# Performance work log

Measured on AMD Instinct MI355X. Metric: run time of the kernel, lower is better.

The kernel has to match this reference:

```python
import jax, jax.numpy as jnp
import numpy as np

N = 100_000   # nodes
E = 1_250_000 # edges
D = 64        # node feature dim
H = 64        # hidden_channels
C = 10        # num_classes
G = 128       # graphs in batch


def setup_inputs() -> dict:
    key = jax.random.key(0)
    ks = jax.random.split(key, 12)
    x = jax.random.normal(ks[0], (N, D), dtype=jnp.float32)
    edge_index = jax.random.randint(ks[1], (2, E), 0, N, dtype=jnp.int64)
    batch = jnp.sort(jax.random.randint(ks[2], (N,), 0, G, dtype=jnp.int64))
    s = lambda fan_in: 1.0 / np.sqrt(fan_in)
    W1 = jax.random.normal(ks[3], (D, H), dtype=jnp.float32) * s(D)
    b1 = jnp.zeros((H,), dtype=jnp.float32)
    W2 = jax.random.normal(ks[4], (H, H), dtype=jnp.float32) * s(H)
    b2 = jnp.zeros((H,), dtype=jnp.float32)
    W3 = jax.random.normal(ks[5], (H, H), dtype=jnp.float32) * s(H)
    b3 = jnp.zeros((H,), dtype=jnp.float32)
    Wl = jax.random.normal(ks[6], (H, C), dtype=jnp.float32) * s(H)
    bl = jnp.zeros((C,), dtype=jnp.float32)
    return {"x": x, "edge_index": edge_index, "batch": batch,
            "W1": W1, "b1": b1, "W2": W2, "b2": b2,
            "W3": W3, "b3": b3, "Wl": Wl, "bl": bl}


def _gcn_conv(h, W, b, src, dst, norm, n_nodes):
    # GCNConv: out[i] = sum_{e: dst(e)=i} norm_e * (h @ W)[src(e)] + b
    h = h @ W
    msg = h[src] * norm[:, None]                       # [E+N, H]
    return jax.ops.segment_sum(msg, dst, num_segments=n_nodes) + b


def reference(x, edge_index, batch, W1, b1, W2, b2, W3, b3, Wl, bl):
    x = x.astype(jnp.float32)
    ei = edge_index.astype(jnp.int64)
    # add self-loops (as PyG gcn_norm does by default)
    loop = jnp.arange(N, dtype=ei.dtype)
    src = jnp.concatenate([ei[0], loop])
    dst = jnp.concatenate([ei[1], loop])
    # symmetric normalization: deg over targets (in-degree incl. self-loops)
    deg = jax.ops.segment_sum(jnp.ones_like(src, dtype=jnp.float32), dst,
                              num_segments=N)
    dinv = jnp.where(deg > 0, jax.lax.rsqrt(jnp.maximum(deg, 1.0)), 0.0)
    norm = dinv[src] * dinv[dst]                       # [E+N]

    h = jax.nn.relu(_gcn_conv(x, W1, b1, src, dst, norm, N))
    h = jax.nn.relu(_gcn_conv(h, W2, b2, src, dst, norm, N))
    h = _gcn_conv(h, W3, b3, src, dst, norm, N)

    # global_mean_pool over graph ids
    ones = jnp.ones((N,), dtype=jnp.float32)
    counts = jax.ops.segment_sum(ones, batch, num_segments=G)
    sums = jax.ops.segment_sum(h, batch, num_segments=G)
    pooled = sums / jnp.maximum(counts, 1.0)[:, None]  # [G, H]

    # dropout is identity in eval mode
    return pooled @ Wl + bl                            # [G, C]
```

## Files before the change

kernel.cpp:

```cpp
#include <hip/hip_runtime.h>
#include <hip/hip_bf16.h>


#define BSHIFT 7
#define BNODES (1 << BSHIFT)
#define EPB    8192
#define MAXDEG 8192
#define MAXBUCKET 32768

typedef __attribute__((ext_vector_type(8))) short bf16x8;
typedef __attribute__((ext_vector_type(4))) float f32x4;

__device__ __forceinline__ void atomAddF(float* p, float v) {
#if defined(__gfx90a__) || defined(__gfx940__) || defined(__gfx941__) || defined(__gfx942__) || defined(__gfx950__)
    unsafeAtomicAdd(p, v);
#else
    atomicAdd(p, v);
#endif
}

__device__ __forceinline__ unsigned short f2bf(float x) {
    unsigned u = __float_as_uint(x);
    u += 0x7FFFu + ((u >> 16) & 1u);
    return (unsigned short)(u >> 16);
}
__device__ __forceinline__ float bf2f(unsigned short b) {
    return __uint_as_float((unsigned)b << 16);
}

__global__ __launch_bounds__(256)
void k_bhist(const int* __restrict__ dst, int* __restrict__ cnt_all,
             int nE, int nBuckets, int binBlocks,
             const float* __restrict__ W1, const float* __restrict__ W2,
             const float* __restrict__ W3, unsigned short* __restrict__ Wt) {
    if (blockIdx.x >= binBlocks) {
        int li = blockIdx.x - binBlocks;
        const float* W = (li == 0) ? W1 : ((li == 1) ? W2 : W3);
        unsigned short* o = Wt + li * 4096;
        for (int idx = threadIdx.x; idx < 4096; idx += 256) {
            int h = idx >> 6, k = idx & 63;
            o[idx] = f2bf(W[k * 64 + h]);
        }
        return;
    }
    __shared__ int cnt[1024];
    const int t = threadIdx.x;
    const int blk = blockIdx.x * EPB;
    for (int b = t; b < nBuckets; b += 256) cnt[b] = 0;
    __syncthreads();
#pragma unroll 4
    for (int i = 0; i < EPB / 256; i++) {
        int e = blk + i * 256 + t;
        if (e < nE) atomicAdd(&cnt[dst[e] >> BSHIFT], 1);
    }
    __syncthreads();
    for (int b = t; b < nBuckets; b += 256)
        cnt_all[(size_t)blockIdx.x * nBuckets + b] = cnt[b];
}

__global__ __launch_bounds__(256)
void k_colscan(int* __restrict__ cnt_all, int* __restrict__ bcnt,
               int nBlocks, int nBuckets) {
    const int lane = threadIdx.x & 63;
    const int b = blockIdx.x * 4 + (threadIdx.x >> 6);
    if (b >= nBuckets) return;
    int running = 0;
    for (int c = 0; c < nBlocks; c += 64) {
        int blk = c + lane;
        int v = (blk < nBlocks) ? cnt_all[(size_t)blk * nBuckets + b] : 0;
        int incl = v;
#pragma unroll
        for (int off = 1; off < 64; off <<= 1) {
            int tv = __shfl_up(incl, off);
            if (lane >= off) incl += tv;
        }
        if (blk < nBlocks) cnt_all[(size_t)blk * nBuckets + b] = running + (incl - v);
        running += __shfl(incl, 63);
    }
    if (lane == 0) bcnt[b] = running;
}

__global__ void k_bscan(const int* __restrict__ bcnt, int* __restrict__ bbase,
                        int nb, int nE) {
    __shared__ int s[256];
    const int t = threadIdx.x;
    const int base = t * 4;
    int v0 = (base + 0 < nb) ? bcnt[base + 0] : 0;
    int v1 = (base + 1 < nb) ? bcnt[base + 1] : 0;
    int v2 = (base + 2 < nb) ? bcnt[base + 2] : 0;
    int v3 = (base + 3 < nb) ? bcnt[base + 3] : 0;
    int tsum = v0 + v1 + v2 + v3;
    s[t] = tsum;
    __syncthreads();
    for (int off = 1; off < 256; off <<= 1) {
        int val = 0;
        if (t >= off) val = s[t - off];
        __syncthreads();
        if (t >= off) s[t] += val;
        __syncthreads();
    }
    int excl = s[t] - tsum;
    if (base + 0 < nb) bbase[base + 0] = excl;
    if (base + 1 < nb) bbase[base + 1] = excl + v0;
    if (base + 2 < nb) bbase[base + 2] = excl + v0 + v1;
    if (base + 3 < nb) bbase[base + 3] = excl + v0 + v1 + v2;
    if (t == 0) bbase[nb] = nE;
}

__global__ __launch_bounds__(256)
void k_bucket(const int* __restrict__ src, const int* __restrict__ dst,
              const int* __restrict__ bbase, const int* __restrict__ cnt_all,
              int* __restrict__ staging, int nE, int nBuckets) {
    __shared__ int cnt[1024];
    __shared__ int lbase[1024];
    const int t = threadIdx.x;
    const int blk = blockIdx.x * EPB;

    for (int b = t; b < nBuckets; b += 256) {
        lbase[b] = bbase[b] + cnt_all[(size_t)blockIdx.x * nBuckets + b];
        cnt[b] = 0;
    }
    __syncthreads();
#pragma unroll 4
    for (int i = 0; i < EPB / 256; i++) {
        int e = blk + i * 256 + t;
        if (e < nE) {
            int s0 = src[e], d0 = dst[e];
            int b = d0 >> BSHIFT;
            int off = atomicAdd(&cnt[b], 1);
            int pos = lbase[b] + off;
            if ((unsigned)pos < (unsigned)nE)
                staging[pos] = (s0 << BSHIFT) | (d0 & (BNODES - 1));
        }
    }
}

__global__ __launch_bounds__(256)
void k_sort(const int* __restrict__ staging, const int* __restrict__ bbase,
            int* __restrict__ csr_s, int* __restrict__ rowptr,
            int* __restrict__ rowend, float* __restrict__ dinv,
            int n, int nE) {
    __shared__ int c[BNODES];
    __shared__ int sc[BNODES];
    __shared__ int cur[BNODES];
    const int t = threadIdx.x;
    const int b = blockIdx.x;
    const int node0 = b << BSHIFT;

    int seg0 = bbase[b];
    int seg1 = bbase[b + 1];
    seg0 = max(0, min(seg0, nE));
    seg1 = max(seg0, min(seg1, nE));
    seg1 = min(seg1, seg0 + MAXBUCKET);

    if (t < BNODES) c[t] = 0;
    __syncthreads();
    for (int e = seg0 + t; e < seg1; e += 256)
        atomicAdd(&c[staging[e] & (BNODES - 1)], 1);
    __syncthreads();
    if (t < BNODES) sc[t] = c[t];
    __syncthreads();
    for (int off = 1; off < BNODES; off <<= 1) {
        int v = 0;
        if (t >= off && t < BNODES) v = sc[t - off];
        __syncthreads();
        if (t >= off && t < BNODES) sc[t] += v;
        __syncthreads();
    }
    if (t < BNODES) {
        int excl = sc[t] - c[t];
        cur[t] = excl;
        int node = node0 + t;
        if (node < n) {
            rowptr[node] = seg0 + excl;
            rowend[node] = seg0 + excl + c[t];
            dinv[node]   = rsqrtf((float)c[t] + 1.0f);
        }
    }
    __syncthreads();
    for (int e = seg0 + t; e < seg1; e += 256) {
        int p = staging[e];
        int l = p & (BNODES - 1);
        int pos = seg0 + atomicAdd(&cur[l], 1);
        if ((unsigned)pos < (unsigned)nE)
            csr_s[pos] = ((unsigned)p) >> BSHIFT;
    }
}

__global__ __launch_bounds__(256)
void k_wfill(const int* __restrict__ csr_s, const float* __restrict__ dinv,
             float* __restrict__ csr_w, int nE, int n) {
    int e = blockIdx.x * blockDim.x + threadIdx.x;
    if (e < nE) {
        int s = csr_s[e];
        s = max(0, min(s, n - 1));
        csr_w[e] = dinv[s];
    }
}

template<bool RELU, typename AT>
__global__ __launch_bounds__(256)
void k_gemm(const AT* __restrict__ in, const unsigned short* __restrict__ Wt,
            const float* __restrict__ bias, unsigned short* __restrict__ out, int n) {
    const int lane = threadIdx.x & 63;
    const int wid  = threadIdx.x >> 6;
    const int col  = lane & 15;
    const int quad = lane >> 4;
    const int node0w = blockIdx.x * 64 + wid * 16;
    const int nodeA  = node0w + col;
    const bool validA = nodeA < n;

    f32x4 zero4 = {0.f, 0.f, 0.f, 0.f};
    f32x4 acc0 = zero4, acc1 = zero4, acc2 = zero4, acc3 = zero4;

#pragma unroll
    for (int ks = 0; ks < 64; ks += 32) {
        const int kb = ks + quad * 8;
        float a[8];
        if constexpr (sizeof(AT) == 4) {
            float4 a0 = make_float4(0.f, 0.f, 0.f, 0.f);
            float4 a1 = make_float4(0.f, 0.f, 0.f, 0.f);
            if (validA) {
                a0 = *(const float4*)((const float*)in + (size_t)nodeA * 64 + kb);
                a1 = *(const float4*)((const float*)in + (size_t)nodeA * 64 + kb + 4);
            }
            a[0] = a0.x; a[1] = a0.y; a[2] = a0.z; a[3] = a0.w;
            a[4] = a1.x; a[5] = a1.y; a[6] = a1.z; a[7] = a1.w;
        } else {
            ushort4 h0 = make_ushort4(0, 0, 0, 0), h1 = make_ushort4(0, 0, 0, 0);
            if (validA) {
                h0 = *(const ushort4*)((const unsigned short*)in + (size_t)nodeA * 64 + kb);
                h1 = *(const ushort4*)((const unsigned short*)in + (size_t)nodeA * 64 + kb + 4);
            }
            a[0] = bf2f(h0.x); a[1] = bf2f(h0.y); a[2] = bf2f(h0.z); a[3] = bf2f(h0.w);
            a[4] = bf2f(h1.x); a[5] = bf2f(h1.y); a[6] = bf2f(h1.z); a[7] = bf2f(h1.w);
        }
        if (RELU) {
#pragma unroll
            for (int i = 0; i < 8; i++) a[i] = fmaxf(a[i] + bias[kb + i], 0.f);
        }
        bf16x8 af;
#pragma unroll
        for (int i = 0; i < 8; i++) af[i] = (short)f2bf(a[i]);

        const bf16x8 b0f = *(const bf16x8*)(Wt + ((0 * 16 + col) * 64 + kb));
        const bf16x8 b1f = *(const bf16x8*)(Wt + ((1 * 16 + col) * 64 + kb));
        const bf16x8 b2f = *(const bf16x8*)(Wt + ((2 * 16 + col) * 64 + kb));
        const bf16x8 b3f = *(const bf16x8*)(Wt + ((3 * 16 + col) * 64 + kb));
        acc0 = __builtin_amdgcn_mfma_f32_16x16x32_bf16(af, b0f, acc0, 0, 0, 0);
        acc1 = __builtin_amdgcn_mfma_f32_16x16x32_bf16(af, b1f, acc1, 0, 0, 0);
        acc2 = __builtin_amdgcn_mfma_f32_16x16x32_bf16(af, b2f, acc2, 0, 0, 0);
        acc3 = __builtin_amdgcn_mfma_f32_16x16x32_bf16(af, b3f, acc3, 0, 0, 0);
    }

#pragma unroll
    for (int r = 0; r < 4; r++) {
        int nn = node0w + quad * 4 + r;
        if (nn < n) {
            size_t base = (size_t)nn * 64 + col;
            out[base +  0] = f2bf(acc0[r]);
            out[base + 16] = f2bf(acc1[r]);
            out[base + 32] = f2bf(acc2[r]);
            out[base + 48] = f2bf(acc3[r]);
        }
    }
}

template<int LAYER>
__global__ __launch_bounds__(256)
void k_agg(const unsigned short* __restrict__ hW, const int* __restrict__ rowptr,
           const int* __restrict__ rowend, const int* __restrict__ csr_s,
           const float* __restrict__ csr_w, const float* __restrict__ dinv,
           unsigned short* __restrict__ aggb, int n, int nE) {
    const int lane = threadIdx.x & 63;
    const int wid  = threadIdx.x >> 6;
    const int nA = blockIdx.x * 8 + wid * 2;
    const int nB = nA + 1;
    if (nA >= n) return;
    const bool vB = (nB < n);

    int rowA = rowptr[nA], endA = rowend[nA];
    rowA = max(0, min(rowA, nE)); endA = max(rowA, min(endA, nE));
    endA = min(endA, rowA + MAXDEG);
    int rowB = 0, endB = 0;
    if (vB) {
        rowB = rowptr[nB]; endB = rowend[nB];
        rowB = max(0, min(rowB, nE)); endB = max(rowB, min(endB, nE));
        endB = min(endB, rowB + MAXDEG);
    }
    const float diA = dinv[nA];
    const float diB = vB ? dinv[nB] : 0.f;

    float a0 = diA * diA * bf2f(hW[(size_t)nA * 64 + lane]);
    float a1 = 0.f, a2 = 0.f, a3 = 0.f;
    float b0 = vB ? diB * diB * bf2f(hW[(size_t)nB * 64 + lane]) : 0.f;
    float b1 = 0.f, b2 = 0.f, b3 = 0.f;

    int baseA = rowA, baseB = rowB;
    while (baseA < endA || baseB < endB) {
        int mA = max(0, min(32, endA - baseA));
        int mB = max(0, min(32, endB - baseB));
        int   s_l = 0;
        float w_l = 0.f;
        if (lane < 32) {
            if (lane < mA) {
                int e = baseA + lane;
                s_l = csr_s[e];
                w_l = csr_w[e] * diA;
            }
        } else {
            int l2 = lane - 32;
            if (l2 < mB) {
                int e = baseB + l2;
                s_l = csr_s[e];
                w_l = csr_w[e] * diB;
            }
        }
        const int m = max(mA, mB);
        int j = 0;
        for (; j + 4 <= m; j += 4) {
            int   sA0 = __shfl(s_l, j),      sA1 = __shfl(s_l, j + 1);
            int   sA2 = __shfl(s_l, j + 2),  sA3 = __shfl(s_l, j + 3);
            int   sB0 = __shfl(s_l, j + 32), sB1 = __shfl(s_l, j + 33);
            int   sB2 = __shfl(s_l, j + 34), sB3 = __shfl(s_l, j + 35);
            float wA0 = __shfl(w_l, j),      wA1 = __shfl(w_l, j + 1);
            float wA2 = __shfl(w_l, j + 2),  wA3 = __shfl(w_l, j + 3);
            float wB0 = __shfl(w_l, j + 32), wB1 = __shfl(w_l, j + 33);
            float wB2 = __shfl(w_l, j + 34), wB3 = __shfl(w_l, j + 35);
            float hA0 = bf2f(hW[(size_t)sA0 * 64 + lane]);
            float hA1 = bf2f(hW[(size_t)sA1 * 64 + lane]);
            float hA2 = bf2f(hW[(size_t)sA2 * 64 + lane]);
            float hA3 = bf2f(hW[(size_t)sA3 * 64 + lane]);
            float hB0 = bf2f(hW[(size_t)sB0 * 64 + lane]);
            float hB1 = bf2f(hW[(size_t)sB1 * 64 + lane]);
            float hB2 = bf2f(hW[(size_t)sB2 * 64 + lane]);
            float hB3 = bf2f(hW[(size_t)sB3 * 64 + lane]);
            a0 += wA0 * hA0; a1 += wA1 * hA1;
            a2 += wA2 * hA2; a3 += wA3 * hA3;
            b0 += wB0 * hB0; b1 += wB1 * hB1;
            b2 += wB2 * hB2; b3 += wB3 * hB3;
        }
        for (; j < m; j++) {
            int   sA = __shfl(s_l, j);
            float wA = __shfl(w_l, j);
            int   sB = __shfl(s_l, j + 32);
            float wB = __shfl(w_l, j + 32);
            a0 += wA * bf2f(hW[(size_t)sA * 64 + lane]);
            b0 += wB * bf2f(hW[(size_t)sB * 64 + lane]);
        }
        baseA += mA;
        baseB += mB;
    }
    aggb[(size_t)nA * 64 + lane] = f2bf((a0 + a1) + (a2 + a3));
    if (vB) aggb[(size_t)nB * 64 + lane] = f2bf((b0 + b1) + (b2 + b3));
}


__global__ void k_pool(const unsigned short* __restrict__ aggb,
                       const int* __restrict__ batch,
                       float* __restrict__ pool, float* __restrict__ cnt, int n) {
    const int lane = threadIdx.x;
    const int base = blockIdx.x * 64;
    int g_cur = -1, run = 0;
    float acc = 0.f;
    for (int j = 0; j < 64; j++) {
        int node = base + j;
        if (node >= n) break;
        int g = batch[node];
        if (g != g_cur) {
            if (g_cur >= 0) {
                atomAddF(&pool[g_cur * 64 + lane], acc);
                if (lane == 0) atomAddF(&cnt[g_cur], (float)run);
            }
            g_cur = g; acc = 0.f; run = 0;
        }
        acc += bf2f(aggb[(size_t)node * 64 + lane]);
        run++;
    }
    if (g_cur >= 0) {
        atomAddF(&pool[g_cur * 64 + lane], acc);
        if (lane == 0) atomAddF(&cnt[g_cur], (float)run);
    }
}

__global__ void k_final(const float* __restrict__ pool, const float* __restrict__ cnt,
                        const float* __restrict__ b3, const float* __restrict__ Wl,
                        const float* __restrict__ bl, float* __restrict__ out) {
    __shared__ float s[64];
    const int g = blockIdx.x, t = threadIdx.x;
    float c = fmaxf(cnt[g], 1.0f);
    s[t] = pool[g * 64 + t] / c + b3[t];
    __syncthreads();
    if (t < 10) {
        float acc = bl[t];
#pragma unroll
        for (int k = 0; k < 64; k++) acc += s[k] * Wl[k * 10 + t];
        out[g * 10 + t] = acc;
    }
}

extern "C" void kernel_launch(void* const* d_in, const int* in_sizes, int n_in,
                              void* d_out, int out_size, void* d_ws, size_t ws_size,
                              hipStream_t stream) {
    const float* x   = (const float*)d_in[0];
    const int*   ei  = (const int*)d_in[1];
    const int*   bat = (const int*)d_in[2];
    const float* W1  = (const float*)d_in[3];
    const float* b1  = (const float*)d_in[4];
    const float* W2  = (const float*)d_in[5];
    const float* b2  = (const float*)d_in[6];
    const float* W3  = (const float*)d_in[7];
    const float* b3  = (const float*)d_in[8];
    const float* Wl  = (const float*)d_in[9];
    const float* bl  = (const float*)d_in[10];
    float* out = (float*)d_out;

    const int N_ = in_sizes[0] / 64;
    const int E_ = in_sizes[1] / 2;
    const int G_ = out_size / 10;
    const int NB_ = (N_ + BNODES - 1) >> BSHIFT;
    const int bin_blocks = (E_ + EPB - 1) / EPB;

    char* p = (char*)d_ws;
    int*   staging = (int*)p;   p += (size_t)E_ * 4;
    int*   csr_s  = (int*)p;    p += (size_t)E_ * 4;
    float* csr_w  = (float*)p;  p += (size_t)E_ * 4;
    unsigned short* aggb = (unsigned short*)p; p += (size_t)N_ * 64 * 2;
    unsigned short* hW   = (unsigned short*)p; p += (size_t)N_ * 64 * 2;
    float* dinv   = (float*)p;  p += (size_t)N_ * 4;
    int*   rowptr = (int*)p;    p += (size_t)N_ * 4;
    int*   rowend = (int*)p;    p += (size_t)N_ * 4;
    float* pool   = (float*)p;  p += (size_t)G_ * 64 * 4;
    float* cnt    = (float*)p;  p += (size_t)G_ * 4;
    unsigned short* Wt = (unsigned short*)p; p += 3 * 4096 * 2;
    int*   bcnt   = (int*)p;    p += (size_t)(NB_ + 1) * 4;
    int*   bbase  = (int*)p;    p += (size_t)(NB_ + 1) * 4;
    int*   cnt_all = (int*)p;   p += (size_t)bin_blocks * NB_ * 4;

    const int* srcp = ei;
    const int* dstp = ei + E_;

    hipMemsetAsync(pool, 0, (size_t)(G_ * 64 + G_) * 4, stream);

    k_bhist<<<bin_blocks + 3, 256, 0, stream>>>(dstp, cnt_all, E_, NB_,
                                                bin_blocks, W1, W2, W3, Wt);
    k_colscan<<<(NB_ + 3) / 4, 256, 0, stream>>>(cnt_all, bcnt, bin_blocks, NB_);
    k_bscan<<<1, 256, 0, stream>>>(bcnt, bbase, NB_, E_);
    k_bucket<<<bin_blocks, 256, 0, stream>>>(srcp, dstp, bbase, cnt_all,
                                             staging, E_, NB_);
    k_sort<<<NB_, 256, 0, stream>>>(staging, bbase, csr_s, rowptr, rowend,
                                    dinv, N_, E_);
    k_wfill<<<(E_ + 255) / 256, 256, 0, stream>>>(csr_s, dinv, csr_w, E_, N_);

    const int gemm_blocks = (N_ + 63) / 64;
    const int agg_blocks  = (N_ + 7) / 8;

    k_gemm<false, float><<<gemm_blocks, 256, 0, stream>>>(x, Wt, nullptr, hW, N_);
    k_agg<1><<<agg_blocks, 256, 0, stream>>>(hW, rowptr, rowend, csr_s, csr_w,
                                             dinv, aggb, N_, E_);
    k_gemm<true, unsigned short><<<gemm_blocks, 256, 0, stream>>>(aggb, Wt + 4096,
                                                                  b1, hW, N_);
    k_agg<2><<<agg_blocks, 256, 0, stream>>>(hW, rowptr, rowend, csr_s, csr_w,
                                             dinv, aggb, N_, E_);
    k_gemm<true, unsigned short><<<gemm_blocks, 256, 0, stream>>>(aggb, Wt + 8192,
                                                                  b2, hW, N_);
    k_agg<3><<<agg_blocks, 256, 0, stream>>>(hW, rowptr, rowend, csr_s, csr_w,
                                             dinv, aggb, N_, E_);

    k_pool<<<(N_ + 63) / 64, 64, 0, stream>>>(aggb, bat, pool, cnt, N_);
    k_final<<<G_, 64, 0, stream>>>(pool, cnt, b3, Wl, bl, out);
}
```

Before: 345.8 us.

## Fuse pool zeroing, weight fill with first GEMM, and pooling into last aggregation

Moves the pool/count zeroing into an extra block of the histogram kernel, merges the per-edge weight fill with the first GEMM into one launch, and folds global mean pooling into the final aggregation kernel via per-node atomics. This removes a memset, two kernel launches and the write/read of the final node features. In exchange, pooling now issues one atomic per node per feature into a small set of graph slots, which can cause heavy atomic contention compared to the earlier run-length reduction.

Measured after the change: 813.2 us. +135.1%, slower.

```diff
diff --git a/kernel.cpp b/kernel.cpp
--- a/kernel.cpp
+++ b/kernel.cpp
@@ -32,14 +32,19 @@
 void k_bhist(const int* __restrict__ dst, int* __restrict__ cnt_all,
              int nE, int nBuckets, int binBlocks,
              const float* __restrict__ W1, const float* __restrict__ W2,
-             const float* __restrict__ W3, unsigned short* __restrict__ Wt) {
+             const float* __restrict__ W3, unsigned short* __restrict__ Wt,
+             float* __restrict__ pool, int poolN) {
     if (blockIdx.x >= binBlocks) {
         int li = blockIdx.x - binBlocks;
-        const float* W = (li == 0) ? W1 : ((li == 1) ? W2 : W3);
-        unsigned short* o = Wt + li * 4096;
-        for (int idx = threadIdx.x; idx < 4096; idx += 256) {
-            int h = idx >> 6, k = idx & 63;
-            o[idx] = f2bf(W[k * 64 + h]);
+        if (li < 3) {
+            const float* W = (li == 0) ? W1 : ((li == 1) ? W2 : W3);
+            unsigned short* o = Wt + li * 4096;
+            for (int idx = threadIdx.x; idx < 4096; idx += 256) {
+                int h = idx >> 6, k = idx & 63;
+                o[idx] = f2bf(W[k * 64 + h]);
+            }
+        } else {
+            for (int i = threadIdx.x; i < poolN; i += 256) pool[i] = 0.f;
         }
         return;
     }
@@ -187,26 +192,17 @@
     }
 }
 
-__global__ __launch_bounds__(256)
-void k_wfill(const int* __restrict__ csr_s, const float* __restrict__ dinv,
-             float* __restrict__ csr_w, int nE, int n) {
-    int e = blockIdx.x * blockDim.x + threadIdx.x;
-    if (e < nE) {
-        int s = csr_s[e];
-        s = max(0, min(s, n - 1));
-        csr_w[e] = dinv[s];
-    }
-}
-
 template<bool RELU, typename AT>
-__global__ __launch_bounds__(256)
-void k_gemm(const AT* __restrict__ in, const unsigned short* __restrict__ Wt,
-            const float* __restrict__ bias, unsigned short* __restrict__ out, int n) {
+__device__ __forceinline__
+void gemm_body(int bid, const AT* __restrict__ in,
+               const unsigned short* __restrict__ Wt,
+               const float* __restrict__ bias,
+               unsigned short* __restrict__ out, int n) {
     const int lane = threadIdx.x & 63;
     const int wid  = threadIdx.x >> 6;
     const int col  = lane & 15;
     const int quad = lane >> 4;
-    const int node0w = blockIdx.x * 64 + wid * 16;
+    const int node0w = bid * 64 + wid * 16;
     const int nodeA  = node0w + col;
     const bool validA = nodeA < n;
 
@@ -266,12 +262,37 @@
     }
 }
 
-template<int LAYER>
+template<bool RELU, typename AT>
+__global__ __launch_bounds__(256)
+void k_gemm(const AT* __restrict__ in, const unsigned short* __restrict__ Wt,
+            const float* __restrict__ bias, unsigned short* __restrict__ out, int n) {
+    gemm_body<RELU, AT>(blockIdx.x, in, Wt, bias, out, n);
+}
+
+__global__ __launch_bounds__(256)
+void k_wfgemm1(const int* __restrict__ csr_s, const float* __restrict__ dinv,
+               float* __restrict__ csr_w, int nE, int n, int wfB,
+               const float* __restrict__ x, const unsigned short* __restrict__ Wt,
+               unsigned short* __restrict__ hW) {
+    if (blockIdx.x < wfB) {
+        int e = blockIdx.x * 256 + threadIdx.x;
+        if (e < nE) {
+            int s = csr_s[e];
+            s = max(0, min(s, n - 1));
+            csr_w[e] = dinv[s];
+        }
+        return;
+    }
+    gemm_body<false, float>(blockIdx.x - wfB, x, Wt, nullptr, hW, n);
+}
+
+template<int LAYER, bool POOL>
 __global__ __launch_bounds__(256)
 void k_agg(const unsigned short* __restrict__ hW, const int* __restrict__ rowptr,
            const int* __restrict__ rowend, const int* __restrict__ csr_s,
            const float* __restrict__ csr_w, const float* __restrict__ dinv,
-           unsigned short* __restrict__ aggb, int n, int nE) {
+           unsigned short* __restrict__ aggb, const int* __restrict__ batch,
+           float* __restrict__ pool, float* __restrict__ cnt, int n, int nE) {
     const int lane = threadIdx.x & 63;
     const int wid  = threadIdx.x >> 6;
     const int nA = blockIdx.x * 8 + wid * 2;
@@ -351,35 +372,20 @@
         baseA += mA;
         baseB += mB;
     }
-    aggb[(size_t)nA * 64 + lane] = f2bf((a0 + a1) + (a2 + a3));
-    if (vB) aggb[(size_t)nB * 64 + lane] = f2bf((b0 + b1) + (b2 + b3));
-}
-
-
-__global__ void k_pool(const unsigned short* __restrict__ aggb,
-                       const int* __restrict__ batch,
-                       float* __restrict__ pool, float* __restrict__ cnt, int n) {
-    const int lane = threadIdx.x;
-    const int base = blockIdx.x * 64;
-    int g_cur = -1, run = 0;
-    float acc = 0.f;
-    for (int j = 0; j < 64; j++) {
-        int node = base + j;
-        if (node >= n) break;
-        int g = batch[node];
-        if (g != g_cur) {
-            if (g_cur >= 0) {
-                atomAddF(&pool[g_cur * 64 + lane], acc);
-                if (lane == 0) atomAddF(&cnt[g_cur], (float)run);
-            }
-            g_cur = g; acc = 0.f; run = 0;
-        }
-        acc += bf2f(aggb[(size_t)node * 64 + lane]);
-        run++;
-    }
-    if (g_cur >= 0) {
-        atomAddF(&pool[g_cur * 64 + lane], acc);
-        if (lane == 0) atomAddF(&cnt[g_cur], (float)run);
+    float vA = (a0 + a1) + (a2 + a3);
+    float vBv = (b0 + b1) + (b2 + b3);
+    if (POOL) {
+        int gA = batch[nA];
+        atomAddF(&pool[(size_t)gA * 64 + lane], vA);
+        if (lane == 0) atomAddF(&cnt[gA], 1.0f);
+        if (vB) {
+            int gB = batch[nB];
+            atomAddF(&pool[(size_t)gB * 64 + lane], vBv);
+            if (lane == 0) atomAddF(&cnt[gB], 1.0f);
+        }
+    } else {
+        aggb[(size_t)nA * 64 + lane] = f2bf(vA);
+        if (vB) aggb[(size_t)nB * 64 + lane] = f2bf(vBv);
     }
 }
 
@@ -440,33 +446,34 @@
     const int* srcp = ei;
     const int* dstp = ei + E_;
 
-    hipMemsetAsync(pool, 0, (size_t)(G_ * 64 + G_) * 4, stream);
-
-    k_bhist<<<bin_blocks + 3, 256, 0, stream>>>(dstp, cnt_all, E_, NB_,
-                                                bin_blocks, W1, W2, W3, Wt);
+    k_bhist<<<bin_blocks + 4, 256, 0, stream>>>(dstp, cnt_all, E_, NB_,
+                                                bin_blocks, W1, W2, W3, Wt,
+                                                pool, G_ * 64 + G_);
     k_colscan<<<(NB_ + 3) / 4, 256, 0, stream>>>(cnt_all, bcnt, bin_blocks, NB_);
     k_bscan<<<1, 256, 0, stream>>>(bcnt, bbase, NB_, E_);
     k_bucket<<<bin_blocks, 256, 0, stream>>>(srcp, dstp, bbase, cnt_all,
                                              staging, E_, NB_);
     k_sort<<<NB_, 256, 0, stream>>>(staging, bbase, csr_s, rowptr, rowend,
                                     dinv, N_, E_);
-    k_wfill<<<(E_ + 255) / 256, 256, 0, stream>>>(csr_s, dinv, csr_w, E_, N_);
 
     const int gemm_blocks = (N_ + 63) / 64;
     const int agg_blocks  = (N_ + 7) / 8;
-
-    k_gemm<false, float><<<gemm_blocks, 256, 0, stream>>>(x, Wt, nullptr, hW, N_);
-    k_agg<1><<<agg_blocks, 256, 0, stream>>>(hW, rowptr, rowend, csr_s, csr_w,
-                                             dinv, aggb, N_, E_);
+    const int wf_blocks   = (E_ + 255) / 256;
+
+    k_wfgemm1<<<wf_blocks + gemm_blocks, 256, 0, stream>>>(
+        csr_s, dinv, csr_w, E_, N_, wf_blocks, x, Wt, hW);
+    k_agg<1, false><<<agg_blocks, 256, 0, stream>>>(hW, rowptr, rowend, csr_s,
+                                                    csr_w, dinv, aggb, bat,
+                                                    pool, cnt, N_, E_);
     k_gemm<true, unsigned short><<<gemm_blocks, 256, 0, stream>>>(aggb, Wt + 4096,
                                                                   b1, hW, N_);
-    k_agg<2><<<agg_blocks, 256, 0, stream>>>(hW, rowptr, rowend, csr_s, csr_w,
-                                             dinv, aggb, N_, E_);
+    k_agg<2, false><<<agg_blocks, 256, 0, stream>>>(hW, rowptr, rowend, csr_s,
+                                                    csr_w, dinv, aggb, bat,
+                                                    pool, cnt, N_, E_);
     k_gemm<true, unsigned short><<<gemm_blocks, 256, 0, stream>>>(aggb, Wt + 8192,
                                                                   b2, hW, N_);
-    k_agg<3><<<agg_blocks, 256, 0, stream>>>(hW, rowptr, rowend, csr_s, csr_w,
-                                             dinv, aggb, N_, E_);
-
-    k_pool<<<(N_ + 63) / 64, 64, 0, stream>>>(aggb, bat, pool, cnt, N_);
+    k_agg<3, true><<<agg_blocks, 256, 0, stream>>>(hW, rowptr, rowend, csr_s,
+                                                   csr_w, dinv, aggb, bat,
+                                                   pool, cnt, N_, E_);
     k_final<<<G_, 64, 0, stream>>>(pool, cnt, b3, Wl, bl, out);
 }
```
